# Kernel tuning notes

Hardware: AMD Instinct MI355X
Metric: run time of the kernel (lower is better)

## Reference

```python
import jax, jax.numpy as jnp
import numpy as np

N_NODES = 100000
N_EDGES = 1600000
NFEATS, NHIDS, NOUT = 128, 128, 64


def _gcn_conv(x, W, b, src, dst, n_nodes):
    # PyG GCNConv: linear transform, then symmetric-normalized aggregation
    # over A + I (self-loops added), then bias.
    h = x @ W                                        # [N, out]
    loop = jnp.arange(n_nodes, dtype=src.dtype)
    s = jnp.concatenate([src, loop])                 # [E + N]
    d = jnp.concatenate([dst, loop])                 # [E + N]
    deg = jax.ops.segment_sum(jnp.ones_like(d, dtype=h.dtype), d,
                              num_segments=n_nodes)  # degree of A + I
    dinv = jnp.where(deg > 0, jax.lax.rsqrt(deg), 0.0)
    norm = dinv[s] * dinv[d]                         # [E + N]
    msg = h[s] * norm[:, None]                       # gather + scale
    out = jax.ops.segment_sum(msg, d, num_segments=n_nodes)  # scatter-add
    return out + b


def setup_inputs() -> dict:
    key = jax.random.key(0)
    k1, k2, k3, k4 = jax.random.split(key, 4)
    edge_index = jax.random.randint(k1, (2, N_EDGES), 0, N_NODES, dtype=jnp.int64)
    x = jax.random.normal(k2, (N_NODES, NFEATS), dtype=jnp.float32)
    W1 = jax.random.normal(k3, (NFEATS, NHIDS), dtype=jnp.float32) / np.sqrt(NFEATS)
    b1 = jnp.zeros((NHIDS,), dtype=jnp.float32)
    W2 = jax.random.normal(k4, (NHIDS, NOUT), dtype=jnp.float32) / np.sqrt(NHIDS)
    b2 = jnp.zeros((NOUT,), dtype=jnp.float32)
    return {"edge_index": edge_index, "x": x, "W1": W1, "b1": b1,
            "W2": W2, "b2": b2}


def reference(edge_index, x, W1, b1, W2, b2):
    src, dst = edge_index[0], edge_index[1]
    n = x.shape[0]
    h = jax.nn.relu(_gcn_conv(x, W1, b1, src, dst, n))
    # dropout(p=0.5, train=False) is the identity in eval mode
    out = _gcn_conv(h, W2, b2, src, dst, n)
    return out
```

## Files before the change

kernel.cpp:

```cpp
#include <hip/hip_runtime.h>
#include <cstdint>
#include <cstddef>

#define NFEATS 128
#define NHIDS  128
#define NOUT   64
#define SB     256
#define CHUNK  4096

using bf16x8 = __attribute__((ext_vector_type(8))) short;
using f32x4  = __attribute__((ext_vector_type(4))) float;

__device__ inline unsigned short f2bf(float f) {
    union { float f; unsigned int u; } v; v.f = f;
    unsigned int r = (v.u + 0x7FFFu + ((v.u >> 16) & 1u)) >> 16;
    return (unsigned short)r;
}
__device__ inline float bflo(unsigned int u) { return __uint_as_float(u << 16); }
__device__ inline float bfhi(unsigned int u) { return __uint_as_float(u & 0xFFFF0000u); }

__global__ void detect_kernel(const void* p, int* flag, long long n_nodes) {
    const long long* q = (const long long*)p;
    long long v = q[threadIdx.x];
    int bad = (v < 0 || v >= n_nodes) ? 1 : 0;
    unsigned long long m = __ballot(bad);
    if (threadIdx.x == 0) *flag = (m != 0ULL) ? 1 : 0;
}

__global__ void hist_kernel(const void* __restrict__ edges, const int* __restrict__ flag,
                            int* __restrict__ histT, int ne, int nch, int nbkt) {
    __shared__ int h[1024];
    int c = blockIdx.x, t = threadIdx.x;
    for (int i = t; i < nbkt; i += 512) h[i] = 0;
    __syncthreads();
    int beg = c * CHUNK, end = min(ne, beg + CHUNK);
    bool is32 = (*flag != 0);
    for (int i = beg + t; i < end; i += 512) {
        int d = is32 ? ((const int*)edges)[ne + i]
                     : (int)((const long long*)edges)[ne + i];
        atomicAdd(&h[d >> 8], 1);
    }
    __syncthreads();
    for (int i = t; i < nbkt; i += 512)
        histT[i * nch + c] = h[i];
}

__global__ void scan_block(const int* __restrict__ v, int* __restrict__ incl,
                           int* __restrict__ partial, int n) {
    __shared__ int sh[256];
    int t = threadIdx.x;
    int i = blockIdx.x * 256 + t;
    sh[t] = (i < n) ? v[i] : 0;
    __syncthreads();
    for (int off = 1; off < 256; off <<= 1) {
        int add = (t >= off) ? sh[t - off] : 0;
        __syncthreads();
        sh[t] += add;
        __syncthreads();
    }
    if (i < n) incl[i] = sh[t];
    if (t == 255) partial[blockIdx.x] = sh[255];
}

__global__ void scan_partials(int* partial, int nb) {
    __shared__ int sh[512];
    __shared__ int carry;
    int t = threadIdx.x;
    if (t == 0) carry = 0;
    __syncthreads();
    for (int base = 0; base < nb; base += 512) {
        int idx = base + t;
        sh[t] = (idx < nb) ? partial[idx] : 0;
        __syncthreads();
        for (int off = 1; off < 512; off <<= 1) {
            int add = (t >= off) ? sh[t - off] : 0;
            __syncthreads();
            sh[t] += add;
            __syncthreads();
        }
        int excl = carry + ((t == 0) ? 0 : sh[t - 1]);
        if (idx < nb) partial[idx] = excl;
        __syncthreads();
        if (t == 0) carry += sh[511];
        __syncthreads();
    }
}

__global__ void finalize_scan(const int* __restrict__ incl, const int* __restrict__ v,
                              const int* __restrict__ partial,
                              int* __restrict__ excl, int m) {
    int i = blockIdx.x * blockDim.x + threadIdx.x;
    if (i < m) excl[i] = partial[i >> 8] + incl[i] - v[i];
}

__global__ void scatter_chunks(const void* __restrict__ edges, const int* __restrict__ flag,
                               const int* __restrict__ chunk_base,
                               unsigned int* __restrict__ ebuf,
                               int ne, int nch, int nbkt) {
    __shared__ int cur[1024];
    int c = blockIdx.x, t = threadIdx.x;
    for (int i = t; i < nbkt; i += 512) cur[i] = chunk_base[i * nch + c];
    __syncthreads();
    int beg = c * CHUNK, end = min(ne, beg + CHUNK);
    bool is32 = (*flag != 0);
    for (int i = beg + t; i < end; i += 512) {
        int s, d;
        if (is32) {
            s = ((const int*)edges)[i];
            d = ((const int*)edges)[ne + i];
        } else {
            s = (int)((const long long*)edges)[i];
            d = (int)((const long long*)edges)[ne + i];
        }
        int pos = atomicAdd(&cur[d >> 8], 1);
        ebuf[pos] = ((unsigned int)s << 8) | (unsigned int)(d & (SB - 1));
    }
}

__global__ void bucket_finalize(const unsigned int* __restrict__ ebuf,
                                const int* __restrict__ chunk_base,
                                int* __restrict__ row_ptr, float* __restrict__ dinv,
                                int* __restrict__ csr_src,
                                int n, int e, int nch, int nbkt) {
    __shared__ int deg[SB];
    __shared__ int incl[SB];
    __shared__ int cur[SB];
    int b = blockIdx.x, t = threadIdx.x;
    int node0 = b * SB;
    int nn = min(SB, n - node0);
    int base = chunk_base[b * nch];
    int bend = (b == nbkt - 1) ? e : chunk_base[(b + 1) * nch];

    deg[t] = 0;
    __syncthreads();
    for (int i = base + t; i < bend; i += SB)
        atomicAdd(&deg[ebuf[i] & (SB - 1)], 1);
    __syncthreads();

    incl[t] = deg[t];
    __syncthreads();
    for (int off = 1; off < SB; off <<= 1) {
        int add = (t >= off) ? incl[t - off] : 0;
        __syncthreads();
        incl[t] += add;
        __syncthreads();
    }
    int lrow = base + incl[t] - deg[t];
    cur[t] = lrow;
    if (t < nn) {
        row_ptr[node0 + t] = lrow;
        dinv[node0 + t]    = rsqrtf((float)(deg[t] + 1));
    }
    if (b == nbkt - 1 && t == 0) row_ptr[n] = e;
    __syncthreads();

    for (int i = base + t; i < bend; i += SB) {
        unsigned int r = ebuf[i];
        int pos = atomicAdd(&cur[r & (SB - 1)], 1);
        csr_src[pos] = (int)(r >> 8);
    }
}

__global__ void w_pack(const float* __restrict__ W1, unsigned short* __restrict__ Wf1,
                       const float* __restrict__ W2, unsigned short* __restrict__ Wf2) {
    int i = blockIdx.x * blockDim.x + threadIdx.x;
    if (i < 128 * 128) {
        int k = i >> 7, n = i & 127;
        Wf1[(((k >> 3) * 128) + n) * 8 + (k & 7)] = f2bf(W1[i]);
    }
    if (i < 128 * 64) {
        int k = i >> 6, n = i & 63;
        Wf2[(((k >> 3) * 64) + n) * 8 + (k & 7)] = f2bf(W2[i]);
    }
}

template <int NC, bool F32IN>
__launch_bounds__(256)
__global__ void gemm_mfma(const void* __restrict__ Xin,
                          const unsigned short* __restrict__ Wf,
                          const float* __restrict__ dinv,
                          unsigned short* __restrict__ hs, int nrows) {
    constexpr int K = 128;
    __shared__ __align__(16) unsigned short Xl[16 * 128 * 8];

    const int tid  = threadIdx.x;
    const int row0 = blockIdx.x * 128;

    for (int i = tid; i < 128 * 32; i += 256) {
        int r  = i >> 5;
        int c4 = i & 31;
        int gr = row0 + r;
        ushort4 v = make_ushort4(0, 0, 0, 0);
        if (gr < nrows) {
            if (F32IN) {
                float4 f = ((const float4*)((const float*)Xin + (size_t)gr * K))[c4];
                v.x = f2bf(f.x); v.y = f2bf(f.y); v.z = f2bf(f.z); v.w = f2bf(f.w);
            } else {
                v = ((const ushort4*)((const unsigned short*)Xin + (size_t)gr * K))[c4];
            }
        }
        int k   = c4 * 4;
        int grp = k >> 3;
        int j0  = k & 7;
        *(ushort4*)(Xl + ((size_t)grp * 128 + r) * 8 + j0) = v;
    }
    __syncthreads();

    const int wv   = tid >> 6;
    const int lane = tid & 63;
    const int m    = lane & 15;
    const int q    = lane >> 4;

    bf16x8 af[2][4];
#pragma unroll
    for (int h = 0; h < 2; ++h)
#pragma unroll
        for (int kt = 0; kt < 4; ++kt)
            af[h][kt] = *(const bf16x8*)(Xl + (((kt * 4 + q) * 128) + h * 64 + wv * 16 + m) * 8);

    int   rbase[2];
    float dv[2][4];
#pragma unroll
    for (int h = 0; h < 2; ++h) {
        rbase[h] = row0 + h * 64 + wv * 16 + q * 4;
#pragma unroll
        for (int i = 0; i < 4; ++i)
            dv[h][i] = (rbase[h] + i < nrows) ? dinv[rbase[h] + i] : 0.f;
    }

#pragma unroll
    for (int nt = 0; nt < NC / 16; ++nt) {
        bf16x8 bfr[4];
#pragma unroll
        for (int kt = 0; kt < 4; ++kt)
            bfr[kt] = *(const bf16x8*)(Wf + (((size_t)(kt * 4 + q) * NC) + nt * 16 + m) * 8);
#pragma unroll
        for (int h = 0; h < 2; ++h) {
            f32x4 acc = {0.f, 0.f, 0.f, 0.f};
#pragma unroll
            for (int kt = 0; kt < 4; ++kt)
                acc = __builtin_amdgcn_mfma_f32_16x16x32_bf16(af[h][kt], bfr[kt], acc, 0, 0, 0);
#pragma unroll
            for (int i = 0; i < 4; ++i) {
                int g = rbase[h] + i;
                if (g < nrows)
                    hs[(size_t)g * NC + nt * 16 + m] = f2bf(acc[i] * dv[h][i]);
            }
        }
    }
}

template <int F, bool RELU, bool OUTBF>
__launch_bounds__(256)
__global__ void aggregate_bf16(const int* __restrict__ row_ptr,
                               const int* __restrict__ csr_src,
                               const uint4* __restrict__ hsu,
                               const float* __restrict__ dinv,
                               const float* __restrict__ b,
                               void* __restrict__ out, int n) {
    constexpr int TPN = F / 8;
    constexpr int NPB = 256 / TPN;
    int node = blockIdx.x * NPB + threadIdx.x / TPN;
    int t    = threadIdx.x % TPN;
    if (node >= n) return;

    uint4 u = hsu[(size_t)node * TPN + t];
    float a[8];
    a[0] = bflo(u.x); a[1] = bfhi(u.x); a[2] = bflo(u.y); a[3] = bfhi(u.y);
    a[4] = bflo(u.z); a[5] = bfhi(u.z); a[6] = bflo(u.w); a[7] = bfhi(u.w);

    int beg = row_ptr[node], end = row_ptr[node + 1];
    for (int e = beg; e < end; e += 8) {
        int rem = end - e;
        int s[8];
#pragma unroll
        for (int j = 0; j < 8; ++j)
            s[j] = csr_src[e + (j < rem ? j : 0)];
        uint4 v[8];
#pragma unroll
        for (int j = 0; j < 8; ++j)
            v[j] = hsu[(size_t)s[j] * TPN + t];
#pragma unroll
        for (int j = 0; j < 8; ++j) {
            if (j < rem) {
                a[0] += bflo(v[j].x); a[1] += bfhi(v[j].x);
                a[2] += bflo(v[j].y); a[3] += bfhi(v[j].y);
                a[4] += bflo(v[j].z); a[5] += bfhi(v[j].z);
                a[6] += bflo(v[j].w); a[7] += bfhi(v[j].w);
            }
        }
    }

    float dvn = dinv[node];
    float4 b0 = ((const float4*)b)[2 * t];
    float4 b1 = ((const float4*)b)[2 * t + 1];
    float o[8];
    o[0] = a[0] * dvn + b0.x; o[1] = a[1] * dvn + b0.y;
    o[2] = a[2] * dvn + b0.z; o[3] = a[3] * dvn + b0.w;
    o[4] = a[4] * dvn + b1.x; o[5] = a[5] * dvn + b1.y;
    o[6] = a[6] * dvn + b1.z; o[7] = a[7] * dvn + b1.w;
    if (RELU) {
#pragma unroll
        for (int j = 0; j < 8; ++j) o[j] = fmaxf(o[j], 0.f);
    }
    if (OUTBF) {
        uint4 ov;
        ov.x = (unsigned int)f2bf(o[0]) | ((unsigned int)f2bf(o[1]) << 16);
        ov.y = (unsigned int)f2bf(o[2]) | ((unsigned int)f2bf(o[3]) << 16);
        ov.z = (unsigned int)f2bf(o[4]) | ((unsigned int)f2bf(o[5]) << 16);
        ov.w = (unsigned int)f2bf(o[6]) | ((unsigned int)f2bf(o[7]) << 16);
        ((uint4*)out)[(size_t)node * TPN + t] = ov;
    } else {
        float4* op = (float4*)out + (size_t)node * (F / 4) + 2 * t;
        op[0] = make_float4(o[0], o[1], o[2], o[3]);
        op[1] = make_float4(o[4], o[5], o[6], o[7]);
    }
}

extern "C" void kernel_launch(void* const* d_in, const int* in_sizes, int n_in,
                              void* d_out, int out_size, void* d_ws, size_t ws_size,
                              hipStream_t stream) {
    const void*  edge = d_in[0];
    const float* x    = (const float*)d_in[1];
    const float* W1   = (const float*)d_in[2];
    const float* b1   = (const float*)d_in[3];
    const float* W2   = (const float*)d_in[4];
    const float* b2   = (const float*)d_in[5];
    float* out = (float*)d_out;

    const int E    = in_sizes[0] / 2;
    const int N    = in_sizes[1] / NFEATS;
    const int NBKT = (N + SB - 1) / SB;
    const int NCH  = (E + CHUNK - 1) / CHUNK;
    const int M    = NBKT * NCH;

    char* w = (char*)d_ws;
    auto carve = [&](size_t bytes) { void* p = w; w += (bytes + 255) & ~(size_t)255; return p; };
    int*            flag       = (int*)           carve(256);
    int*            histT      = (int*)           carve(sizeof(int) * (size_t)M);
    int*            incl       = (int*)           carve(sizeof(int) * (size_t)M);
    int*            partial    = (int*)           carve(sizeof(int) * 4096);
    int*            chunk_base = (int*)           carve(sizeof(int) * (size_t)M);
    int*            row_ptr    = (int*)           carve(sizeof(int) * ((size_t)N + 1));
    float*          dinv       = (float*)         carve(sizeof(float) * (size_t)N);
    unsigned int*   ebuf       = (unsigned int*)  carve(sizeof(int) * (size_t)E);
    int*            csr_src    = (int*)           carve(sizeof(int) * (size_t)E);
    unsigned short* Wf1        = (unsigned short*)carve(2 * (size_t)NFEATS * NHIDS);
    unsigned short* Wf2        = (unsigned short*)carve(2 * (size_t)NHIDS * NOUT);
    unsigned short* hs1        = (unsigned short*)carve(2 * (size_t)N * NHIDS);
    unsigned short* h1         = (unsigned short*)carve(2 * (size_t)N * NHIDS);
    unsigned short* hs2        = (unsigned short*)carve(2 * (size_t)N * NOUT);

    const int B   = 256;
    const int nbS = (M + 255) / 256;

    detect_kernel<<<1, 64, 0, stream>>>(edge, flag, (long long)N);

    hist_kernel<<<NCH, 512, 0, stream>>>(edge, flag, histT, E, NCH, NBKT);
    scan_block<<<nbS, 256, 0, stream>>>(histT, incl, partial, M);
    scan_partials<<<1, 512, 0, stream>>>(partial, nbS);
    finalize_scan<<<nbS, 256, 0, stream>>>(incl, histT, partial, chunk_base, M);
    scatter_chunks<<<NCH, 512, 0, stream>>>(edge, flag, chunk_base, ebuf, E, NCH, NBKT);
    bucket_finalize<<<NBKT, SB, 0, stream>>>(ebuf, chunk_base, row_ptr, dinv, csr_src,
                                             N, E, NCH, NBKT);

    w_pack<<<(128 * 128 + B - 1) / B, B, 0, stream>>>(W1, Wf1, W2, Wf2);

    gemm_mfma<NHIDS, true><<<(N + 127) / 128, B, 0, stream>>>(x, Wf1, dinv, hs1, N);
    {
        constexpr int NPB = 256 / (NHIDS / 8);
        aggregate_bf16<NHIDS, true, true><<<(N + NPB - 1) / NPB, B, 0, stream>>>(
            row_ptr, csr_src, (const uint4*)hs1, dinv, b1, h1, N);
    }

    gemm_mfma<NOUT, false><<<(N + 127) / 128, B, 0, stream>>>(h1, Wf2, dinv, hs2, N);
    {
        constexpr int NPB = 256 / (NOUT / 8);
        aggregate_bf16<NOUT, false, false><<<(N + NPB - 1) / NPB, B, 0, stream>>>(
            row_ptr, csr_src, (const uint4*)hs2, dinv, b2, out, N);
    }
}
```

Baseline: 278.0 us.

## Software-pipeline aggregation gathers with cooperative CSR index loads and shuffles

```diff
diff --git a/kernel.cpp b/kernel.cpp
--- a/kernel.cpp
+++ b/kernel.cpp
@@ -10,6 +10,7 @@
 
 using bf16x8 = __attribute__((ext_vector_type(8))) short;
 using f32x4  = __attribute__((ext_vector_type(4))) float;
+using u32x4  = __attribute__((ext_vector_type(4))) unsigned int;
 
 __device__ inline unsigned short f2bf(float f) {
     union { float f; unsigned int u; } v; v.f = f;
@@ -258,11 +259,15 @@
                                const float* __restrict__ dinv,
                                const float* __restrict__ b,
                                void* __restrict__ out, int n) {
-    constexpr int TPN = F / 8;
-    constexpr int NPB = 256 / TPN;
+    constexpr int TPN  = F / 8;
+    constexpr int NPB  = 256 / TPN;
+    constexpr int CH   = 16;
+    constexpr int NCSR = CH / TPN;
     int node = blockIdx.x * NPB + threadIdx.x / TPN;
     int t    = threadIdx.x % TPN;
     if (node >= n) return;
+    const int lane = threadIdx.x & 63;
+    const int gb   = lane & ~(TPN - 1);
 
     uint4 u = hsu[(size_t)node * TPN + t];
     float a[8];
@@ -270,24 +275,73 @@
     a[4] = bflo(u.z); a[5] = bfhi(u.z); a[6] = bflo(u.w); a[7] = bfhi(u.w);
 
     int beg = row_ptr[node], end = row_ptr[node + 1];
-    for (int e = beg; e < end; e += 8) {
-        int rem = end - e;
-        int s[8];
-#pragma unroll
-        for (int j = 0; j < 8; ++j)
-            s[j] = csr_src[e + (j < rem ? j : 0)];
-        uint4 v[8];
-#pragma unroll
-        for (int j = 0; j < 8; ++j)
-            v[j] = hsu[(size_t)s[j] * TPN + t];
-#pragma unroll
-        for (int j = 0; j < 8; ++j) {
-            if (j < rem) {
-                a[0] += bflo(v[j].x); a[1] += bfhi(v[j].x);
-                a[2] += bflo(v[j].y); a[3] += bfhi(v[j].y);
-                a[4] += bflo(v[j].z); a[5] += bfhi(v[j].z);
-                a[6] += bflo(v[j].w); a[7] += bfhi(v[j].w);
-            }
+
+    if (beg < end) {
+        const u32x4* hb = (const u32x4*)hsu;
+        u32x4 v[CH];
+        int sva, svb;
+        int base = beg;
+
+        {
+            const int* pc0 = csr_src + min(base + t, end - 1);
+            asm volatile("global_load_dword %0, %1, off" : "=&v"(sva) : "v"(pc0));
+            if (NCSR == 2) {
+                const int* pc1 = csr_src + min(base + TPN + t, end - 1);
+                asm volatile("global_load_dword %0, %1, off" : "=&v"(svb) : "v"(pc1));
+            }
+        }
+        asm volatile("s_waitcnt vmcnt(0)");
+        __builtin_amdgcn_sched_barrier(0);
+
+        while (true) {
+            int rem = min(CH, end - base);
+
+#pragma unroll
+            for (int j = 0; j < CH; ++j) {
+                int jj = min(j, rem - 1);
+                int sj;
+                if (TPN == 16) {
+                    sj = __shfl(sva, gb + jj, 64);
+                } else {
+                    int s0 = __shfl(sva, gb + (jj & 7), 64);
+                    int s1 = __shfl(svb, gb + (jj & 7), 64);
+                    sj = (jj < 8) ? s0 : s1;
+                }
+                const u32x4* p = hb + (size_t)sj * TPN + t;
+                asm volatile("global_load_dwordx4 %0, %1, off" : "=&v"(v[j]) : "v"(p));
+            }
+
+            int  nbase = base + CH;
+            bool more  = nbase < end;
+            if (more) {
+                const int* pc0 = csr_src + min(nbase + t, end - 1);
+                asm volatile("global_load_dword %0, %1, off" : "=&v"(sva) : "v"(pc0));
+                if (NCSR == 2) {
+                    const int* pc1 = csr_src + min(nbase + TPN + t, end - 1);
+                    asm volatile("global_load_dword %0, %1, off" : "=&v"(svb) : "v"(pc1));
+                }
+                if (NCSR == 1) asm volatile("s_waitcnt vmcnt(1)");
+                else           asm volatile("s_waitcnt vmcnt(2)");
+            } else {
+                asm volatile("s_waitcnt vmcnt(0)");
+            }
+            __builtin_amdgcn_sched_barrier(0);
+
+#pragma unroll
+            for (int j = 0; j < CH; ++j) {
+                if (j < rem) {
+                    unsigned int x0 = v[j][0], x1 = v[j][1], x2 = v[j][2], x3 = v[j][3];
+                    a[0] += bflo(x0); a[1] += bfhi(x0);
+                    a[2] += bflo(x1); a[3] += bfhi(x1);
+                    a[4] += bflo(x2); a[5] += bfhi(x2);
+                    a[6] += bflo(x3); a[7] += bfhi(x3);
+                }
+            }
+
+            if (!more) break;
+            base = nbase;
+            asm volatile("s_waitcnt vmcnt(0)");
+            __builtin_amdgcn_sched_barrier(0);
         }
     }
 
```

Measured after the change: 279.4 us. No clear change (+0.5%).
